# Kernel tuning notes

Measured on AMD Instinct MI355X. Metric: run time of the kernel, lower is better.

## Reference

```python
import jax, jax.numpy as jnp
import numpy as np

HIDDEN = 1024
HEADS = 16
HEAD_DIM = HIDDEN // HEADS          # 64
ROT = 2 * (HEAD_DIM // 3 // 2)      # 20 (d/h/w rotary chunk), residual = 4
GRID = 256 // 16                    # crop_size // patch_size = 16
DEPTH = 16 // 2                     # frames_per_clip // tubelet_size = 8
N_VIDEO = DEPTH * GRID * GRID       # 2048
N_ACTION = 16
B = 2
SCALE = HEAD_DIM ** -0.5


def _rope(x, pos):
    # interleaved RoPE (VJEPA2 rotate_queries_or_keys): pairs (x[2i], x[2i+1])
    D = x.shape[-1]
    omega = 1.0 / (10000.0 ** (jnp.arange(D // 2, dtype=x.dtype) / (D / 2.0)))
    freq = pos.astype(x.dtype)[..., None] * omega          # (N, D/2)
    cos, sin = jnp.cos(freq), jnp.sin(freq)
    x1, x2 = x[..., 0::2], x[..., 1::2]
    return jnp.stack([x1 * cos - x2 * sin, x2 * cos + x1 * sin], axis=-1).reshape(x.shape)


def _rope3(qk, d_pos, h_pos, w_pos):
    # rotate three ROT-sized chunks (depth/height/width axes), leave residual dims as-is
    parts = [_rope(qk[..., 0:ROT], d_pos),
             _rope(qk[..., ROT:2 * ROT], h_pos),
             _rope(qk[..., 2 * ROT:3 * ROT], w_pos)]
    if 3 * ROT < HEAD_DIM:
        parts.append(qk[..., 3 * ROT:])
    return jnp.concatenate(parts, axis=-1)


def _forward(video_hidden_states, action_hidden_states, W_q, b_q, W_k, b_k, W_v, b_v,
             W_qa, b_qa, W_ka, b_ka, W_va, b_va, W_proj, b_proj, W_proj_a, b_proj_a):
    Bsz, Nv, _ = video_hidden_states.shape
    Na = action_hidden_states.shape[1]

    def proj(x, W, b):  # -> (B, H, N, Dh)
        y = x @ W.T + b
        return y.reshape(Bsz, -1, HEADS, HEAD_DIM).transpose(0, 2, 1, 3)

    qv = proj(video_hidden_states, W_q, b_q)
    kv = proj(video_hidden_states, W_k, b_k)
    vv = proj(video_hidden_states, W_v, b_v)

    # 3-axis position ids for raster-ordered video tokens
    ids = jnp.arange(Nv)
    tpf = GRID * GRID
    d_pos = ids // tpf
    rem = ids - tpf * d_pos
    h_pos = rem // GRID
    w_pos = rem - GRID * h_pos

    qv = _rope3(qv, d_pos, h_pos, w_pos)
    kv = _rope3(kv, d_pos, h_pos, w_pos)

    qa = proj(action_hidden_states, W_qa, b_qa)
    ka = proj(action_hidden_states, W_ka, b_ka)
    va = proj(action_hidden_states, W_va, b_va)

    # actions: linspace between frame-id of token 0 and token 1 (faithful to source)
    a_pos = jnp.linspace(d_pos[0].astype(jnp.float32), d_pos[1].astype(jnp.float32), Na)
    qa = _rope3(qa, a_pos, a_pos, a_pos)
    ka = _rope3(ka, a_pos, a_pos, a_pos)

    # joint attention over concatenated video+action token sequence
    q = jnp.concatenate([qv, qa], axis=2)
    k = jnp.concatenate([kv, ka], axis=2)
    v = jnp.concatenate([vv, va], axis=2)

    scores = jnp.einsum('bhqd,bhkd->bhqk', q, k) * SCALE
    probs = jax.nn.softmax(scores, axis=-1)
    ctx = jnp.einsum('bhqk,bhkd->bhqd', probs, v)
    ctx = ctx.transpose(0, 2, 1, 3).reshape(Bsz, Nv + Na, HIDDEN)

    out_video = ctx[:, :Nv] @ W_proj.T + b_proj
    out_action = ctx[:, Nv:] @ W_proj_a.T + b_proj_a
    return out_video, out_action


def setup_inputs() -> dict:
    key = jax.random.key(0)
    ks = jax.random.split(key, 12)
    sd = HIDDEN ** -0.5
    inp = {}
    for i, n in enumerate(['q', 'k', 'v', 'qa', 'ka', 'va', 'proj', 'proj_a']):
        inp[f'W_{n}'] = jax.random.normal(ks[i], (HIDDEN, HIDDEN), jnp.float32) * sd
        inp[f'b_{n}'] = jnp.zeros((HIDDEN,), jnp.float32)
    inp['video_hidden_states'] = jax.random.normal(ks[10], (B, N_VIDEO, HIDDEN), jnp.float32)
    inp['action_hidden_states'] = jax.random.normal(ks[11], (B, N_ACTION, HIDDEN), jnp.float32)
    return inp


def reference(video_hidden_states, action_hidden_states, W_q, b_q, W_k, b_k, W_v, b_v,
              W_qa, b_qa, W_ka, b_ka, W_va, b_va, W_proj, b_proj, W_proj_a, b_proj_a):
    return _forward(video_hidden_states, action_hidden_states, W_q, b_q, W_k, b_k, W_v, b_v,
                    W_qa, b_qa, W_ka, b_ka, W_va, b_va, W_proj, b_proj, W_proj_a, b_proj_a)
```

## Files before the change

### kernel.cpp

```cpp
#include <hip/hip_runtime.h>
#include <stdint.h>

#define HID   1024
#define NHEAD 16
#define HDIM  64
#define NV    2048
#define NA    16
#define NTOK  2064
#define BSZ   2
#define MROWS 4128
#define WSZ   1048576
#define EXP_C1 0.18033688011112042f
#define EXP_C2 16.0f

typedef __bf16 bf16x8 __attribute__((ext_vector_type(8)));
typedef unsigned short u16x8 __attribute__((ext_vector_type(8)));
typedef unsigned short u16x4 __attribute__((ext_vector_type(4)));
typedef float f32x4 __attribute__((ext_vector_type(4)));

__device__ __forceinline__ unsigned short f2bf(float f) {
  unsigned u = __builtin_bit_cast(unsigned, f);
  u += 0x7FFFu + ((u >> 16) & 1u);
  return (unsigned short)(u >> 16);
}
__device__ __forceinline__ unsigned short f2bf_trunc(float f) {
  return (unsigned short)(__builtin_bit_cast(unsigned, f) >> 16);
}
__device__ __forceinline__ void async_copy16(const void* g, void* l) {
  __builtin_amdgcn_global_load_lds(
      (const __attribute__((address_space(1))) unsigned int*)g,
      (__attribute__((address_space(3))) unsigned int*)l, 16, 0, 0);
}

__global__ __launch_bounds__(256) void cvt_kernel(
    const float* __restrict__ W0, const float* __restrict__ W1,
    const float* __restrict__ W2, const float* __restrict__ W3,
    const float* __restrict__ W4, const float* __restrict__ W5,
    const float* __restrict__ W6, const float* __restrict__ W7,
    const float* __restrict__ video, const float* __restrict__ action,
    unsigned short* __restrict__ Wb, unsigned short* __restrict__ Xb)
{
  const int y = blockIdx.y;
  const size_t idx = ((size_t)blockIdx.x * 256 + threadIdx.x) * 8;
  const float* src; unsigned short* dst;
  if      (y == 0)  { src = W0; dst = Wb; }
  else if (y == 1)  { src = W1; dst = Wb + 1 * WSZ; }
  else if (y == 2)  { src = W2; dst = Wb + 2 * WSZ; }
  else if (y == 3)  { src = W3; dst = Wb + 3 * WSZ; }
  else if (y == 4)  { src = W4; dst = Wb + 4 * WSZ; }
  else if (y == 5)  { src = W5; dst = Wb + 5 * WSZ; }
  else if (y == 6)  { src = W6; dst = Wb + 6 * WSZ; }
  else if (y == 7)  { src = W7; dst = Wb + 7 * WSZ; }
  else if (y < 12)  { src = video + (size_t)(y - 8) * WSZ; dst = Xb + (size_t)(y - 8) * WSZ; }
  else              { if (idx >= (size_t)BSZ * NA * HID) return;
                      src = action; dst = Xb + (size_t)4096 * HID; }
  float4 f0 = *(const float4*)(src + idx);
  float4 f1 = *(const float4*)(src + idx + 4);
  u16x8 v;
  v[0]=f2bf(f0.x); v[1]=f2bf(f0.y); v[2]=f2bf(f0.z); v[3]=f2bf(f0.w);
  v[4]=f2bf(f1.x); v[5]=f2bf(f1.y); v[6]=f2bf(f1.z); v[7]=f2bf(f1.w);
  *(u16x8*)(dst + idx) = v;
}

__device__ __forceinline__ void row2bt(int rg, int& b, int& tok, bool& valid) {
  if (rg < 4096) { b = rg >> 11; tok = rg & 2047; valid = true; }
  else { int t = rg - 4096; b = t >> 4; tok = 2048 + (t & 15); valid = rg < MROWS; }
}

__global__ __launch_bounds__(256) void qkv128_kernel(
    const unsigned short* __restrict__ Xb, const unsigned short* __restrict__ Wb,
    const float* __restrict__ bq, const float* __restrict__ bk,
    const float* __restrict__ bv, const float* __restrict__ bqa,
    const float* __restrict__ bka, const float* __restrict__ bva,
    unsigned short* __restrict__ Qo, unsigned short* __restrict__ Ko,
    unsigned short* __restrict__ Vt)
{
  __shared__ unsigned short As[128 * 32];
  __shared__ unsigned short Bs[128 * 32];

  const int tid  = threadIdx.x;
  const int w    = tid >> 6;
  const int l    = tid & 63;
  const int quad = l >> 4;
  const int l16  = l & 15;
  const int lrow = l >> 2;
  const int lk   = (l & 3) * 8;
  const int z    = blockIdx.z;
  const int m0   = blockIdx.y * 128;
  const int n0   = blockIdx.x * 128;
  const bool atile = (blockIdx.y == 32);

  const unsigned short* Wm = Wb + (size_t)(atile ? 3 + z : z) * WSZ;
  const float* bias = (z == 0) ? (atile ? bqa : bq)
                    : (z == 1) ? (atile ? bka : bk)
                               : (atile ? bva : bv);

  const int am = (w & 1) * 64;
  const int bn = (w >> 1) * 64;

  f32x4 acc[4][4] = {};

  for (int kt = 0; kt < HID; kt += 32) {
    __syncthreads();
#pragma unroll
    for (int i = 0; i < 2; i++) {
      int trow = w * 32 + i * 16;
      int arow = min(m0 + trow + lrow, MROWS - 1);
      async_copy16(Xb + (size_t)arow * HID + kt + lk, &As[trow * 32]);
      async_copy16(Wm + (size_t)(n0 + trow + lrow) * HID + kt + lk, &Bs[trow * 32]);
    }
    __syncthreads();

    bf16x8 af[4], bf[4];
#pragma unroll
    for (int mi = 0; mi < 4; mi++)
      af[mi] = __builtin_bit_cast(bf16x8, *(const u16x8*)&As[(am + mi * 16 + l16) * 32 + quad * 8]);
#pragma unroll
    for (int ni = 0; ni < 4; ni++)
      bf[ni] = __builtin_bit_cast(bf16x8, *(const u16x8*)&Bs[(bn + ni * 16 + l16) * 32 + quad * 8]);
#pragma unroll
    for (int mi = 0; mi < 4; mi++)
#pragma unroll
      for (int ni = 0; ni < 4; ni++)
        acc[mi][ni] = __builtin_amdgcn_mfma_f32_16x16x32_bf16(af[mi], bf[ni], acc[mi][ni], 0, 0, 0);
  }

  if (z < 2) {
    unsigned short* O = (z == 0) ? Qo : Ko;
#pragma unroll
    for (int mi = 0; mi < 4; mi++) {
      const int rgb = m0 + am + mi * 16 + quad * 4;
#pragma unroll
      for (int ni = 0; ni < 4; ni++) {
        const int gcol = n0 + bn + ni * 16 + l16;
        const int head = gcol >> 6, col = gcol & 63;
        const float bias_v = bias[gcol];
        const int seg = (col >= 40) ? 2 : (col >= 20) ? 1 : 0;
        const int tin = col - seg * 20;
        const float om = exp2f(-(float)(tin >> 1) * 1.3287712379549449f);
        const bool evn = !(tin & 1);
#pragma unroll
        for (int r = 0; r < 4; r++) {
          int rg = rgb + r;
          int b, tok; bool valid;
          row2bt(rg, b, tok, valid);
          float val = acc[mi][ni][r] + bias_v;
          float part = __shfl_xor(val, 1);
          if (tok < 2048 && col < 60) {
            int dp = tok >> 8, hp = (tok >> 4) & 15, wp = tok & 15;
            float pos = (seg == 0) ? (float)dp : (seg == 1) ? (float)hp : (float)wp;
            float fr = pos * om;
            float cs = cosf(fr), sn = sinf(fr);
            val = evn ? (val * cs - part * sn) : (val * cs + part * sn);
          }
          if (valid)
            O[(((size_t)b * NHEAD + head) * NTOK + tok) * HDIM + col] = f2bf(val);
        }
      }
    }
  } else {
#pragma unroll
    for (int mi = 0; mi < 4; mi++) {
      const int rgb = m0 + am + mi * 16 + quad * 4;
      int b, tok; bool valid;
      row2bt(rgb, b, tok, valid);
#pragma unroll
      for (int ni = 0; ni < 4; ni++) {
        const int gcol = n0 + bn + ni * 16 + l16;
        const int head = gcol >> 6, d = gcol & 63;
        const float bias_v = bias[gcol];
        u16x4 pk;
#pragma unroll
        for (int r = 0; r < 4; r++) pk[r] = f2bf(acc[mi][ni][r] + bias_v);
        if (valid)
          *(u16x4*)&Vt[(((size_t)b * NHEAD + head) * HDIM + d) * NTOK + tok] = pk;
      }
    }
  }
}

__global__ __launch_bounds__(256) void attn_kernel(
    const unsigned short* __restrict__ Q,
    const unsigned short* __restrict__ K,
    const unsigned short* __restrict__ Vt,
    unsigned short* __restrict__ ctx)
{
  __shared__ unsigned short Qs[64][72];
  __shared__ unsigned short Ks[64][72];
  __shared__ unsigned short Vts[64][72];
  __shared__ unsigned short Ps[4][16][68];

  const int tid  = threadIdx.x;
  const int wave = tid >> 6;
  const int lane = tid & 63;
  const int quad = lane >> 4;
  const int l16  = lane & 15;
  const int bh   = blockIdx.y;
  const int q0   = blockIdx.x * 64;
  const unsigned short* Qp  = Q  + (size_t)bh * NTOK * HDIM;
  const unsigned short* Kp  = K  + (size_t)bh * NTOK * HDIM;
  const unsigned short* Vtp = Vt + (size_t)bh * HDIM * NTOK;

  const int r  = tid >> 2;
  const int c0 = (tid & 3) * 8;

  {
    int row = min(q0 + r, NTOK - 1);
#pragma unroll
    for (int cc = 0; cc < 2; cc++) {
      int c = c0 + cc * 32;
      *(u16x8*)&Qs[r][c] = *(const u16x8*)(Qp + (size_t)row * HDIM + c);
    }
  }

  u16x8 ones_u;
#pragma unroll
  for (int i = 0; i < 8; i++) ones_u[i] = 0x3F80;
  const bf16x8 ones = __builtin_bit_cast(bf16x8, ones_u);

  f32x4 oacc[4] = {};
  f32x4 lacc = {};

  for (int kv0 = 0; kv0 < NTOK; kv0 += 64) {
    __syncthreads();
    {
      int row = min(kv0 + r, NTOK - 1);
#pragma unroll
      for (int cc = 0; cc < 2; cc++) {
        int c = c0 + cc * 32;
        *(u16x8*)&Ks[r][c]  = *(const u16x8*)(Kp + (size_t)row * HDIM + c);
        *(u16x8*)&Vts[r][c] = *(const u16x8*)(Vtp + (size_t)r * NTOK + kv0 + c);
      }
    }
    __syncthreads();

    f32x4 sacc[4] = {};
#pragma unroll
    for (int kq = 0; kq < 64; kq += 32) {
      bf16x8 a = __builtin_bit_cast(bf16x8, *(const u16x8*)&Qs[wave * 16 + l16][kq + quad * 8]);
#pragma unroll
      for (int nt = 0; nt < 4; nt++) {
        bf16x8 bb = __builtin_bit_cast(bf16x8, *(const u16x8*)&Ks[nt * 16 + l16][kq + quad * 8]);
        sacc[nt] = __builtin_amdgcn_mfma_f32_16x16x32_bf16(a, bb, sacc[nt], 0, 0, 0);
      }
    }

#pragma unroll
    for (int nt = 0; nt < 4; nt++) {
      bool valid = (kv0 + nt * 16 + l16) < NTOK;
#pragma unroll
      for (int rr = 0; rr < 4; rr++) {
        float p = exp2f(__builtin_fmaf(sacc[nt][rr], EXP_C1, -EXP_C2));
        p = valid ? p : 0.f;
        Ps[wave][quad * 4 + rr][nt * 16 + l16] = f2bf_trunc(p);
      }
    }

#pragma unroll
    for (int kq = 0; kq < 64; kq += 32) {
      u16x4 alo = *(const u16x4*)&Ps[wave][l16][kq + quad * 8];
      u16x4 ahi = *(const u16x4*)&Ps[wave][l16][kq + quad * 8 + 4];
      bf16x8 a = __builtin_bit_cast(bf16x8,
          __builtin_shufflevector(alo, ahi, 0, 1, 2, 3, 4, 5, 6, 7));
#pragma unroll
      for (int nt = 0; nt < 4; nt++) {
        bf16x8 bb = __builtin_bit_cast(bf16x8, *(const u16x8*)&Vts[nt * 16 + l16][kq + quad * 8]);
        oacc[nt] = __builtin_amdgcn_mfma_f32_16x16x32_bf16(a, bb, oacc[nt], 0, 0, 0);
      }
      lacc = __builtin_amdgcn_mfma_f32_16x16x32_bf16(a, ones, lacc, 0, 0, 0);
    }
  }

  const int b = bh >> 4, h = bh & 15;
  float rl[4];
#pragma unroll
  for (int rr = 0; rr < 4; rr++) rl[rr] = 1.f / lacc[rr];
#pragma unroll
  for (int nt = 0; nt < 4; nt++) {
#pragma unroll
    for (int rr = 0; rr < 4; rr++) {
      int token = q0 + wave * 16 + quad * 4 + rr;
      if (token < NTOK) {
        int row = (token < 2048) ? (b * 2048 + token) : (4096 + b * NA + (token - 2048));
        int d = nt * 16 + l16;
        ctx[(size_t)row * HID + h * HDIM + d] = f2bf(oacc[nt][rr] * rl[rr]);
      }
    }
  }
}

__global__ __launch_bounds__(256) void proj128_kernel(
    const unsigned short* __restrict__ ctx, const unsigned short* __restrict__ Wb,
    const float* __restrict__ bp, const float* __restrict__ bpa,
    float* __restrict__ out)
{
  __shared__ unsigned short As[128 * 32];
  __shared__ unsigned short Bs[128 * 32];

  const int tid  = threadIdx.x;
  const int w    = tid >> 6;
  const int l    = tid & 63;
  const int quad = l >> 4;
  const int l16  = l & 15;
  const int lrow = l >> 2;
  const int lk   = (l & 3) * 8;
  const int m0   = blockIdx.y * 128;
  const int n0   = blockIdx.x * 128;
  const bool atile = (blockIdx.y == 32);

  const unsigned short* Wm = Wb + (size_t)(atile ? 7 : 6) * WSZ;
  const float* bias = atile ? bpa : bp;

  const int am = (w & 1) * 64;
  const int bn = (w >> 1) * 64;

  f32x4 acc[4][4] = {};

  for (int kt = 0; kt < HID; kt += 32) {
    __syncthreads();
#pragma unroll
    for (int i = 0; i < 2; i++) {
      int trow = w * 32 + i * 16;
      int arow = min(m0 + trow + lrow, MROWS - 1);
      async_copy16(ctx + (size_t)arow * HID + kt + lk, &As[trow * 32]);
      async_copy16(Wm + (size_t)(n0 + trow + lrow) * HID + kt + lk, &Bs[trow * 32]);
    }
    __syncthreads();

    bf16x8 af[4], bf[4];
#pragma unroll
    for (int mi = 0; mi < 4; mi++)
      af[mi] = __builtin_bit_cast(bf16x8, *(const u16x8*)&As[(am + mi * 16 + l16) * 32 + quad * 8]);
#pragma unroll
    for (int ni = 0; ni < 4; ni++)
      bf[ni] = __builtin_bit_cast(bf16x8, *(const u16x8*)&Bs[(bn + ni * 16 + l16) * 32 + quad * 8]);
#pragma unroll
    for (int mi = 0; mi < 4; mi++)
#pragma unroll
      for (int ni = 0; ni < 4; ni++)
        acc[mi][ni] = __builtin_amdgcn_mfma_f32_16x16x32_bf16(af[mi], bf[ni], acc[mi][ni], 0, 0, 0);
  }

#pragma unroll
  for (int mi = 0; mi < 4; mi++) {
    const int rgb = m0 + am + mi * 16 + quad * 4;
#pragma unroll
    for (int ni = 0; ni < 4; ni++) {
      const int gcol = n0 + bn + ni * 16 + l16;
      const float bias_v = bias[gcol];
#pragma unroll
      for (int r = 0; r < 4; r++) {
        int rg = rgb + r;
        if (rg < MROWS) out[(size_t)rg * HID + gcol] = acc[mi][ni][r] + bias_v;
      }
    }
  }
}

extern "C" void kernel_launch(void* const* d_in, const int* in_sizes, int n_in,
                              void* d_out, int out_size, void* d_ws, size_t ws_size,
                              hipStream_t stream) {
  const float* A[18];
  if (in_sizes[0] == HID * HID) {
    for (int i = 0; i < 18; i++) A[i] = (const float*)d_in[i];
  } else {
    A[16] = (const float*)d_in[0];
    A[17] = (const float*)d_in[1];
    for (int i = 0; i < 16; i++) A[i] = (const float*)d_in[i + 2];
  }
  const float *Wq = A[0], *bq = A[1], *Wk = A[2], *bk = A[3], *Wv = A[4], *bv = A[5];
  const float *Wqa = A[6], *bqa = A[7], *Wka = A[8], *bka = A[9], *Wva = A[10], *bva = A[11];
  const float *Wp = A[12], *bp = A[13], *Wpa = A[14], *bpa = A[15];
  const float *video = A[16], *action = A[17];
  float* out = (float*)d_out;

  const size_t qkv_elems = (size_t)BSZ * NHEAD * NTOK * HDIM;
  unsigned short* Wb  = (unsigned short*)d_ws;
  unsigned short* Xb  = Wb + (size_t)8 * WSZ;
  unsigned short* Qw  = Xb + (size_t)MROWS * HID;
  unsigned short* Kw  = Qw + qkv_elems;
  unsigned short* Vtw = Kw + qkv_elems;
  unsigned short* ctx = Vtw + qkv_elems;

  dim3 g0(512, 13);
  cvt_kernel<<<g0, 256, 0, stream>>>(Wq, Wk, Wv, Wqa, Wka, Wva, Wp, Wpa,
                                     video, action, Wb, Xb);
  dim3 g1(8, 33, 3);
  qkv128_kernel<<<g1, 256, 0, stream>>>(Xb, Wb, bq, bk, bv, bqa, bka, bva,
                                        Qw, Kw, Vtw);
  dim3 g2(33, BSZ * NHEAD);
  attn_kernel<<<g2, 256, 0, stream>>>(Qw, Kw, Vtw, ctx);
  dim3 g3(8, 33);
  proj128_kernel<<<g3, 256, 0, stream>>>(ctx, Wb, bp, bpa, out);
}
```

Measured before the change: 382.1 us.

## Double-buffer GEMM loads, fuse QKV per head, prefetch attention KV tiles

The QKV GEMM now computes Q, K and V for one head per block, sharing the A tile across all three weight matrices. It also double-buffers the shared-memory loads with async copies issued one step ahead. The projection GEMM is double-buffered with a K-tile of 64. Attention prefetches the next K/V tile into registers, drops the per-element bounds mask for the full 2048-token loop, and handles the 16 action tokens in a separate tail step. Together these are meant to hide global-load latency and cut barriers, at the cost of more shared memory and registers per block.

```diff
diff --git a/kernel.cpp b/kernel.cpp
--- a/kernel.cpp
+++ b/kernel.cpp
@@ -67,7 +67,7 @@
   else { int t = rg - 4096; b = t >> 4; tok = 2048 + (t & 15); valid = rg < MROWS; }
 }
 
-__global__ __launch_bounds__(256) void qkv128_kernel(
+__global__ __launch_bounds__(256, 2) void qkvf_kernel(
     const unsigned short* __restrict__ Xb, const unsigned short* __restrict__ Wb,
     const float* __restrict__ bq, const float* __restrict__ bk,
     const float* __restrict__ bv, const float* __restrict__ bqa,
@@ -75,105 +75,114 @@
     unsigned short* __restrict__ Qo, unsigned short* __restrict__ Ko,
     unsigned short* __restrict__ Vt)
 {
-  __shared__ unsigned short As[128 * 32];
-  __shared__ unsigned short Bs[128 * 32];
+  __shared__ unsigned short As[2][128 * 32];
+  __shared__ unsigned short Bs[2][3][64 * 32];
 
   const int tid  = threadIdx.x;
   const int w    = tid >> 6;
   const int l    = tid & 63;
   const int quad = l >> 4;
   const int l16  = l & 15;
-  const int lrow = l >> 2;
+  const int lr4  = l >> 2;
   const int lk   = (l & 3) * 8;
-  const int z    = blockIdx.z;
+  const int head = blockIdx.x;
+  const int n0   = head * 64;
   const int m0   = blockIdx.y * 128;
-  const int n0   = blockIdx.x * 128;
   const bool atile = (blockIdx.y == 32);
 
-  const unsigned short* Wm = Wb + (size_t)(atile ? 3 + z : z) * WSZ;
-  const float* bias = (z == 0) ? (atile ? bqa : bq)
-                    : (z == 1) ? (atile ? bka : bk)
-                               : (atile ? bva : bv);
-
-  const int am = (w & 1) * 64;
-  const int bn = (w >> 1) * 64;
-
-  f32x4 acc[4][4] = {};
-
-  for (int kt = 0; kt < HID; kt += 32) {
+  const float* biasz[3] = { atile ? bqa : bq, atile ? bka : bk, atile ? bva : bv };
+
+  const unsigned short* pa0 = Xb + (size_t)min(m0 + w * 32 + lr4,      MROWS - 1) * HID + lk;
+  const unsigned short* pa1 = Xb + (size_t)min(m0 + w * 32 + 16 + lr4, MROWS - 1) * HID + lk;
+  const unsigned short* pbz[3];
+#pragma unroll
+  for (int z = 0; z < 3; z++)
+    pbz[z] = Wb + (size_t)(atile ? 3 + z : z) * WSZ + (size_t)(n0 + w * 16 + lr4) * HID + lk;
+
+  f32x4 acc[3][2][4] = {};
+
+  async_copy16(pa0, &As[0][(w * 32) * 32]);
+  async_copy16(pa1, &As[0][(w * 32 + 16) * 32]);
+#pragma unroll
+  for (int z = 0; z < 3; z++) async_copy16(pbz[z], &Bs[0][z][(w * 16) * 32]);
+
+  for (int kt = 0; kt < 32; kt++) {
+    const int cur = kt & 1;
     __syncthreads();
-#pragma unroll
-    for (int i = 0; i < 2; i++) {
-      int trow = w * 32 + i * 16;
-      int arow = min(m0 + trow + lrow, MROWS - 1);
-      async_copy16(Xb + (size_t)arow * HID + kt + lk, &As[trow * 32]);
-      async_copy16(Wm + (size_t)(n0 + trow + lrow) * HID + kt + lk, &Bs[trow * 32]);
-    }
-    __syncthreads();
-
-    bf16x8 af[4], bf[4];
-#pragma unroll
-    for (int mi = 0; mi < 4; mi++)
-      af[mi] = __builtin_bit_cast(bf16x8, *(const u16x8*)&As[(am + mi * 16 + l16) * 32 + quad * 8]);
-#pragma unroll
-    for (int ni = 0; ni < 4; ni++)
-      bf[ni] = __builtin_bit_cast(bf16x8, *(const u16x8*)&Bs[(bn + ni * 16 + l16) * 32 + quad * 8]);
-#pragma unroll
-    for (int mi = 0; mi < 4; mi++)
-#pragma unroll
-      for (int ni = 0; ni < 4; ni++)
-        acc[mi][ni] = __builtin_amdgcn_mfma_f32_16x16x32_bf16(af[mi], bf[ni], acc[mi][ni], 0, 0, 0);
-  }
-
-  if (z < 2) {
-    unsigned short* O = (z == 0) ? Qo : Ko;
-#pragma unroll
-    for (int mi = 0; mi < 4; mi++) {
-      const int rgb = m0 + am + mi * 16 + quad * 4;
+    if (kt < 31) {
+      const int kn = (kt + 1) * 32;
+      async_copy16(pa0 + kn, &As[cur ^ 1][(w * 32) * 32]);
+      async_copy16(pa1 + kn, &As[cur ^ 1][(w * 32 + 16) * 32]);
+#pragma unroll
+      for (int z = 0; z < 3; z++) async_copy16(pbz[z] + kn, &Bs[cur ^ 1][z][(w * 16) * 32]);
+    }
+    bf16x8 af[2];
+#pragma unroll
+    for (int mi = 0; mi < 2; mi++)
+      af[mi] = __builtin_bit_cast(bf16x8, *(const u16x8*)&As[cur][(w * 32 + mi * 16 + l16) * 32 + quad * 8]);
+#pragma unroll
+    for (int z = 0; z < 3; z++) {
 #pragma unroll
       for (int ni = 0; ni < 4; ni++) {
-        const int gcol = n0 + bn + ni * 16 + l16;
-        const int head = gcol >> 6, col = gcol & 63;
-        const float bias_v = bias[gcol];
-        const int seg = (col >= 40) ? 2 : (col >= 20) ? 1 : 0;
-        const int tin = col - seg * 20;
-        const float om = exp2f(-(float)(tin >> 1) * 1.3287712379549449f);
-        const bool evn = !(tin & 1);
-#pragma unroll
-        for (int r = 0; r < 4; r++) {
-          int rg = rgb + r;
-          int b, tok; bool valid;
-          row2bt(rg, b, tok, valid);
-          float val = acc[mi][ni][r] + bias_v;
-          float part = __shfl_xor(val, 1);
-          if (tok < 2048 && col < 60) {
-            int dp = tok >> 8, hp = (tok >> 4) & 15, wp = tok & 15;
-            float pos = (seg == 0) ? (float)dp : (seg == 1) ? (float)hp : (float)wp;
-            float fr = pos * om;
-            float cs = cosf(fr), sn = sinf(fr);
-            val = evn ? (val * cs - part * sn) : (val * cs + part * sn);
+        bf16x8 bb = __builtin_bit_cast(bf16x8, *(const u16x8*)&Bs[cur][z][(ni * 16 + l16) * 32 + quad * 8]);
+#pragma unroll
+        for (int mi = 0; mi < 2; mi++)
+          acc[z][mi][ni] = __builtin_amdgcn_mfma_f32_16x16x32_bf16(af[mi], bb, acc[z][mi][ni], 0, 0, 0);
+      }
+    }
+  }
+
+#pragma unroll
+  for (int z = 0; z < 3; z++) {
+    const float* bias = biasz[z];
+    if (z < 2) {
+      unsigned short* O = (z == 0) ? Qo : Ko;
+#pragma unroll
+      for (int mi = 0; mi < 2; mi++) {
+        const int rgb = m0 + w * 32 + mi * 16 + quad * 4;
+#pragma unroll
+        for (int ni = 0; ni < 4; ni++) {
+          const int col = ni * 16 + l16;
+          const float bias_v = bias[n0 + col];
+          const int seg = (col >= 40) ? 2 : (col >= 20) ? 1 : 0;
+          const int tin = col - seg * 20;
+          const float om = exp2f(-(float)(tin >> 1) * 1.3287712379549449f);
+          const bool evn = !(tin & 1);
+#pragma unroll
+          for (int r = 0; r < 4; r++) {
+            int rg = rgb + r;
+            int b, tok; bool valid;
+            row2bt(rg, b, tok, valid);
+            float val = acc[z][mi][ni][r] + bias_v;
+            float part = __shfl_xor(val, 1);
+            if (tok < 2048 && col < 60) {
+              int dp = tok >> 8, hp = (tok >> 4) & 15, wp = tok & 15;
+              float pos = (seg == 0) ? (float)dp : (seg == 1) ? (float)hp : (float)wp;
+              float fr = pos * om;
+              float cs = cosf(fr), sn = sinf(fr);
+              val = evn ? (val * cs - part * sn) : (val * cs + part * sn);
+            }
+            if (valid)
+              O[(((size_t)b * NHEAD + head) * NTOK + tok) * HDIM + col] = f2bf(val);
           }
+        }
+      }
+    } else {
+#pragma unroll
+      for (int mi = 0; mi < 2; mi++) {
+        const int rgb = m0 + w * 32 + mi * 16 + quad * 4;
+        int b, tok; bool valid;
+        row2bt(rgb, b, tok, valid);
+#pragma unroll
+        for (int ni = 0; ni < 4; ni++) {
+          const int d = ni * 16 + l16;
+          const float bias_v = bias[n0 + d];
+          u16x4 pk;
+#pragma unroll
+          for (int r = 0; r < 4; r++) pk[r] = f2bf(acc[z][mi][ni][r] + bias_v);
           if (valid)
-            O[(((size_t)b * NHEAD + head) * NTOK + tok) * HDIM + col] = f2bf(val);
+            *(u16x4*)&Vt[(((size_t)b * NHEAD + head) * HDIM + d) * NTOK + tok] = pk;
         }
-      }
-    }
-  } else {
-#pragma unroll
-    for (int mi = 0; mi < 4; mi++) {
-      const int rgb = m0 + am + mi * 16 + quad * 4;
-      int b, tok; bool valid;
-      row2bt(rgb, b, tok, valid);
-#pragma unroll
-      for (int ni = 0; ni < 4; ni++) {
-        const int gcol = n0 + bn + ni * 16 + l16;
-        const int head = gcol >> 6, d = gcol & 63;
-        const float bias_v = bias[gcol];
-        u16x4 pk;
-#pragma unroll
-        for (int r = 0; r < 4; r++) pk[r] = f2bf(acc[mi][ni][r] + bias_v);
-        if (valid)
-          *(u16x4*)&Vt[(((size_t)b * NHEAD + head) * HDIM + d) * NTOK + tok] = pk;
       }
     }
   }
@@ -221,18 +230,33 @@
   f32x4 oacc[4] = {};
   f32x4 lacc = {};
 
-  for (int kv0 = 0; kv0 < NTOK; kv0 += 64) {
+  u16x8 kreg[2], vreg[2];
+#pragma unroll
+  for (int cc = 0; cc < 2; cc++) {
+    int c = c0 + cc * 32;
+    kreg[cc] = *(const u16x8*)(Kp + (size_t)r * HDIM + c);
+    vreg[cc] = *(const u16x8*)(Vtp + (size_t)r * NTOK + c);
+  }
+
+  for (int it = 0; it < 32; it++) {
+    const int kv0 = it * 64;
     __syncthreads();
-    {
-      int row = min(kv0 + r, NTOK - 1);
+#pragma unroll
+    for (int cc = 0; cc < 2; cc++) {
+      int c = c0 + cc * 32;
+      *(u16x8*)&Ks[r][c]  = kreg[cc];
+      *(u16x8*)&Vts[r][c] = vreg[cc];
+    }
+    __syncthreads();
+    if (it < 31) {
+      int row = kv0 + 64 + r;
 #pragma unroll
       for (int cc = 0; cc < 2; cc++) {
         int c = c0 + cc * 32;
-        *(u16x8*)&Ks[r][c]  = *(const u16x8*)(Kp + (size_t)row * HDIM + c);
-        *(u16x8*)&Vts[r][c] = *(const u16x8*)(Vtp + (size_t)r * NTOK + kv0 + c);
-      }
-    }
-    __syncthreads();
+        kreg[cc] = *(const u16x8*)(Kp + (size_t)row * HDIM + c);
+        vreg[cc] = *(const u16x8*)(Vtp + (size_t)r * NTOK + kv0 + 64 + c);
+      }
+    }
 
     f32x4 sacc[4] = {};
 #pragma unroll
@@ -246,15 +270,11 @@
     }
 
 #pragma unroll
-    for (int nt = 0; nt < 4; nt++) {
-      bool valid = (kv0 + nt * 16 + l16) < NTOK;
-#pragma unroll
-      for (int rr = 0; rr < 4; rr++) {
-        float p = exp2f(__builtin_fmaf(sacc[nt][rr], EXP_C1, -EXP_C2));
-        p = valid ? p : 0.f;
-        Ps[wave][quad * 4 + rr][nt * 16 + l16] = f2bf_trunc(p);
-      }
-    }
+    for (int nt = 0; nt < 4; nt++)
+#pragma unroll
+      for (int rr = 0; rr < 4; rr++)
+        Ps[wave][quad * 4 + rr][nt * 16 + l16] =
+            f2bf_trunc(exp2f(__builtin_fmaf(sacc[nt][rr], EXP_C1, -EXP_C2)));
 
 #pragma unroll
     for (int kq = 0; kq < 64; kq += 32) {
@@ -269,6 +289,43 @@
       }
       lacc = __builtin_amdgcn_mfma_f32_16x16x32_bf16(a, ones, lacc, 0, 0, 0);
     }
+  }
+
+  __syncthreads();
+  if (tid < 64) {
+    int rr16 = tid >> 2;
+#pragma unroll
+    for (int cc = 0; cc < 2; cc++) {
+      int c = (tid & 3) * 8 + cc * 32;
+      *(u16x8*)&Ks[rr16][c] = *(const u16x8*)(Kp + (size_t)(2048 + rr16) * HDIM + c);
+    }
+  }
+  if ((tid & 3) < 2)
+    *(u16x8*)&Vts[r][(tid & 3) * 8] = *(const u16x8*)(Vtp + (size_t)r * NTOK + 2048 + (tid & 3) * 8);
+  __syncthreads();
+  {
+    f32x4 s0 = {};
+#pragma unroll
+    for (int kq = 0; kq < 64; kq += 32) {
+      bf16x8 a = __builtin_bit_cast(bf16x8, *(const u16x8*)&Qs[wave * 16 + l16][kq + quad * 8]);
+      bf16x8 bb = __builtin_bit_cast(bf16x8, *(const u16x8*)&Ks[l16][kq + quad * 8]);
+      s0 = __builtin_amdgcn_mfma_f32_16x16x32_bf16(a, bb, s0, 0, 0, 0);
+    }
+#pragma unroll
+    for (int rr = 0; rr < 4; rr++) {
+      Ps[wave][quad * 4 + rr][l16]      = f2bf_trunc(exp2f(__builtin_fmaf(s0[rr], EXP_C1, -EXP_C2)));
+      Ps[wave][quad * 4 + rr][16 + l16] = 0;
+    }
+    u16x4 alo = *(const u16x4*)&Ps[wave][l16][quad * 8];
+    u16x4 ahi = *(const u16x4*)&Ps[wave][l16][quad * 8 + 4];
+    bf16x8 a = __builtin_bit_cast(bf16x8,
+        __builtin_shufflevector(alo, ahi, 0, 1, 2, 3, 4, 5, 6, 7));
+#pragma unroll
+    for (int nt = 0; nt < 4; nt++) {
+      bf16x8 bb = __builtin_bit_cast(bf16x8, *(const u16x8*)&Vts[nt * 16 + l16][quad * 8]);
+      oacc[nt] = __builtin_amdgcn_mfma_f32_16x16x32_bf16(a, bb, oacc[nt], 0, 0, 0);
+    }
+    lacc = __builtin_amdgcn_mfma_f32_16x16x32_bf16(a, ones, lacc, 0, 0, 0);
   }
 
   const int b = bh >> 4, h = bh & 15;
@@ -289,21 +346,21 @@
   }
 }
 
-__global__ __launch_bounds__(256) void proj128_kernel(
+__global__ __launch_bounds__(256, 2) void proj128_kernel(
     const unsigned short* __restrict__ ctx, const unsigned short* __restrict__ Wb,
     const float* __restrict__ bp, const float* __restrict__ bpa,
     float* __restrict__ out)
 {
-  __shared__ unsigned short As[128 * 32];
-  __shared__ unsigned short Bs[128 * 32];
+  __shared__ unsigned short As[2][128 * 64];
+  __shared__ unsigned short Bs[2][128 * 64];
 
   const int tid  = threadIdx.x;
   const int w    = tid >> 6;
   const int l    = tid & 63;
   const int quad = l >> 4;
   const int l16  = l & 15;
-  const int lrow = l >> 2;
-  const int lk   = (l & 3) * 8;
+  const int lr8  = l >> 3;
+  const int lk   = (l & 7) * 8;
   const int m0   = blockIdx.y * 128;
   const int n0   = blockIdx.x * 128;
   const bool atile = (blockIdx.y == 32);
@@ -311,34 +368,51 @@
   const unsigned short* Wm = Wb + (size_t)(atile ? 7 : 6) * WSZ;
   const float* bias = atile ? bpa : bp;
 
+  const unsigned short* pa[4];
+  const unsigned short* pb[4];
+#pragma unroll
+  for (int i = 0; i < 4; i++) {
+    pa[i] = ctx + (size_t)min(m0 + w * 32 + i * 8 + lr8, MROWS - 1) * HID + lk;
+    pb[i] = Wm + (size_t)(n0 + w * 32 + i * 8 + lr8) * HID + lk;
+  }
+
   const int am = (w & 1) * 64;
   const int bn = (w >> 1) * 64;
 
   f32x4 acc[4][4] = {};
 
-  for (int kt = 0; kt < HID; kt += 32) {
+#pragma unroll
+  for (int i = 0; i < 4; i++) {
+    async_copy16(pa[i], &As[0][(w * 32 + i * 8) * 64]);
+    async_copy16(pb[i], &Bs[0][(w * 32 + i * 8) * 64]);
+  }
+
+  for (int kt = 0; kt < 16; kt++) {
+    const int cur = kt & 1;
     __syncthreads();
-#pragma unroll
-    for (int i = 0; i < 2; i++) {
-      int trow = w * 32 + i * 16;
-      int arow = min(m0 + trow + lrow, MROWS - 1);
-      async_copy16(ctx + (size_t)arow * HID + kt + lk, &As[trow * 32]);
-      async_copy16(Wm + (size_t)(n0 + trow + lrow) * HID + kt + lk, &Bs[trow * 32]);
-    }
-    __syncthreads();
-
-    bf16x8 af[4], bf[4];
-#pragma unroll
-    for (int mi = 0; mi < 4; mi++)
-      af[mi] = __builtin_bit_cast(bf16x8, *(const u16x8*)&As[(am + mi * 16 + l16) * 32 + quad * 8]);
-#pragma unroll
-    for (int ni = 0; ni < 4; ni++)
-      bf[ni] = __builtin_bit_cast(bf16x8, *(const u16x8*)&Bs[(bn + ni * 16 + l16) * 32 + quad * 8]);
-#pragma unroll
-    for (int mi = 0; mi < 4; mi++)
+    if (kt < 15) {
+      const int kn = (kt + 1) * 64;
+#pragma unroll
+      for (int i = 0; i < 4; i++) {
+        async_copy16(pa[i] + kn, &As[cur ^ 1][(w * 32 + i * 8) * 64]);
+        async_copy16(pb[i] + kn, &Bs[cur ^ 1][(w * 32 + i * 8) * 64]);
+      }
+    }
+#pragma unroll
+    for (int kq = 0; kq < 64; kq += 32) {
+      bf16x8 af[4], bf[4];
+#pragma unroll
+      for (int mi = 0; mi < 4; mi++)
+        af[mi] = __builtin_bit_cast(bf16x8, *(const u16x8*)&As[cur][(am + mi * 16 + l16) * 64 + kq + quad * 8]);
 #pragma unroll
       for (int ni = 0; ni < 4; ni++)
-        acc[mi][ni] = __builtin_amdgcn_mfma_f32_16x16x32_bf16(af[mi], bf[ni], acc[mi][ni], 0, 0, 0);
+        bf[ni] = __builtin_bit_cast(bf16x8, *(const u16x8*)&Bs[cur][(bn + ni * 16 + l16) * 64 + kq + quad * 8]);
+#pragma unroll
+      for (int mi = 0; mi < 4; mi++)
+#pragma unroll
+        for (int ni = 0; ni < 4; ni++)
+          acc[mi][ni] = __builtin_amdgcn_mfma_f32_16x16x32_bf16(af[mi], bf[ni], acc[mi][ni], 0, 0, 0);
+    }
   }
 
 #pragma unroll
@@ -385,9 +459,9 @@
   dim3 g0(512, 13);
   cvt_kernel<<<g0, 256, 0, stream>>>(Wq, Wk, Wv, Wqa, Wka, Wva, Wp, Wpa,
                                      video, action, Wb, Xb);
-  dim3 g1(8, 33, 3);
-  qkv128_kernel<<<g1, 256, 0, stream>>>(Xb, Wb, bq, bk, bv, bqa, bka, bva,
-                                        Qw, Kw, Vtw);
+  dim3 g1(16, 33);
+  qkvf_kernel<<<g1, 256, 0, stream>>>(Xb, Wb, bq, bk, bv, bqa, bka, bva,
+                                      Qw, Kw, Vtw);
   dim3 g2(33, BSZ * NHEAD);
   attn_kernel<<<g2, 256, 0, stream>>>(Qw, Kw, Vtw, ctx);
   dim3 g3(8, 33);
```

Measured after the change: 380.6 us. Within noise of the previous version (-0.4%).
